# Performance work log

Measured on AMD Instinct MI355X. Metric: run time of the kernel, lower is better.

The kernel has to match this reference:

```python
import jax, jax.numpy as jnp
import numpy as np

EPS = 1e-12  # F.normalize default eps


def setup_inputs() -> dict:
    key = jax.random.key(0)
    k1, k2, k3 = jax.random.split(key, 3)
    B, C, H, W = 4, 64, 64, 64
    background = jax.random.normal(k1, (B, C, H, W), dtype=jnp.float32)
    foreground = jax.random.normal(k2, (B, C, H, W), dtype=jnp.float32)
    # binary mask, broadcast over channels
    mask = jnp.round(jax.random.uniform(k3, (B, 1, H, W), dtype=jnp.float32))
    return {"background": background, "foreground": foreground, "mask": mask}


def _l2norm(x, axis):
    # matches torch F.normalize: x / max(||x||, eps)
    n = jnp.sqrt(jnp.sum(x * x, axis=axis, keepdims=True))
    return x / jnp.maximum(n, EPS)


def reference(background, foreground, mask):
    B, C, H, W = background.shape
    bg_flat = background.reshape(B, C, H * W)   # [B, C, K]
    fg_flat = foreground.reshape(B, C, H * W)   # [B, C, Q]
    norm_bg = _l2norm(bg_flat, axis=1)
    norm_fg = _l2norm(fg_flat, axis=1)
    # cosine-similarity scores [B, K, Q]
    attention = jnp.einsum('bck,bcq->bkq', norm_bg, norm_fg)
    attention = jax.nn.softmax(attention, axis=1)  # over bg (key) axis
    attended = jnp.einsum('bck,bkq->bcq', bg_flat, attention)
    attended = attended.reshape(B, C, H, W)
    return foreground * (1.0 - mask) + attended * mask
```

## Files before the change

### kernel.cpp

```cpp
#include <hip/hip_runtime.h>
#include <math.h>

#define CC 64
#define HWN 4096
#define QB 32
#define KSPLIT 4
#define KT 32
#define NCH (HWN / KSPLIT / KT)

typedef __attribute__((ext_vector_type(8))) short bf16x8;
typedef __attribute__((ext_vector_type(4))) float f32x4;

__device__ __align__(16) unsigned short g_bgT[4][HWN][CC];
__device__ __align__(16) unsigned short g_bgN[4][CC][HWN];
__device__ __align__(16) unsigned short g_fgT[4][HWN][CC];

static __device__ __forceinline__ unsigned int f2bf(float x) {
  union { float f; unsigned int u; } v; v.f = x;
  return (v.u + 0x7fffu + ((v.u >> 16) & 1u)) >> 16;
}
static __device__ __forceinline__ unsigned int packbf(float lo, float hi) {
  return f2bf(lo) | (f2bf(hi) << 16);
}

__global__ __launch_bounds__(256) void prep_kernel(const float* __restrict__ bg,
                                                   const float* __restrict__ fg) {
  __shared__ float lds[64 * 65];
  const int bid = blockIdx.x;
  const int kt = bid & 63, b = (bid >> 6) & 3, which = bid >> 8;
  const float* src = (which ? fg : bg) + (size_t)b * CC * HWN + kt * 64;
  const int tid = threadIdx.x;

  {
    int c = tid >> 2, k0 = (tid & 3) * 16;
#pragma unroll
    for (int j4 = 0; j4 < 4; ++j4) {
      float4 v = *(const float4*)(src + (size_t)c * HWN + k0 + 4 * j4);
      lds[(k0 + 4 * j4 + 0) * 65 + c] = v.x;
      lds[(k0 + 4 * j4 + 1) * 65 + c] = v.y;
      lds[(k0 + 4 * j4 + 2) * 65 + c] = v.z;
      lds[(k0 + 4 * j4 + 3) * 65 + c] = v.w;
    }
  }
  __syncthreads();

  const int k = tid >> 2, u = tid & 3;
  float ss = 0.f;
#pragma unroll
  for (int j = 0; j < 16; ++j) {
    float v = lds[k * 65 + u * 16 + j];
    ss = fmaf(v, v, ss);
  }
  ss += __shfl_xor(ss, 1, 64);
  ss += __shfl_xor(ss, 2, 64);
  const float s = 1.0f / fmaxf(sqrtf(ss), 1e-12f);

  {
    unsigned int* gT32 = (unsigned int*)(which ? &g_fgT[0][0][0] : &g_bgT[0][0][0]);
    size_t R = (size_t)b * HWN + kt * 64 + k;
    unsigned int w8[8];
#pragma unroll
    for (int i = 0; i < 8; ++i) {
      int c2 = u * 16 + 2 * i;
      w8[i] = packbf(lds[k * 65 + c2] * s, lds[k * 65 + c2 + 1] * s);
    }
    *(uint4*)&gT32[R * 32 + u * 8]     = make_uint4(w8[0], w8[1], w8[2], w8[3]);
    *(uint4*)&gT32[R * 32 + u * 8 + 4] = make_uint4(w8[4], w8[5], w8[6], w8[7]);
  }

  if (which == 0) {
    unsigned int* gN32 = (unsigned int*)&g_bgN[0][0][0];
    int cN = tid >> 2, vN = tid & 3;
    unsigned int n8[8];
#pragma unroll
    for (int i = 0; i < 8; ++i) {
      int kk = vN * 16 + 2 * i;
      n8[i] = packbf(lds[kk * 65 + cN], lds[(kk + 1) * 65 + cN]);
    }
    size_t RN = ((size_t)b * CC + cN) * (HWN / 2) + kt * 32 + vN * 8;
    *(uint4*)&gN32[RN]     = make_uint4(n8[0], n8[1], n8[2], n8[3]);
    *(uint4*)&gN32[RN + 4] = make_uint4(n8[4], n8[5], n8[6], n8[7]);
  }
}

#define P_OFF 65536
#define ML_OFF 75776
#define SMEM_BYTES 76288
__global__ __launch_bounds__(256, 2) void attn_kernel(const float* __restrict__ fg,
                                                      const float* __restrict__ mask,
                                                      float* __restrict__ out) {
  __shared__ __align__(16) char smem[SMEM_BYTES];
  const int b = blockIdx.y;
  const int q0 = blockIdx.x * QB;
  const int tid = threadIdx.x;
  const int lane = tid & 63;
  const int ks = tid >> 6;
  const int m16 = lane & 15;
  const int quad = lane >> 4;

  bf16x8 Bf[2][2];
#pragma unroll
  for (int qf = 0; qf < 2; ++qf)
#pragma unroll
    for (int h = 0; h < 2; ++h)
      Bf[qf][h] = *(const bf16x8*)&g_fgT[b][q0 + qf * 16 + m16][h * 32 + quad * 8];

  const unsigned short* srcT[4];
  const unsigned short* srcN[4];
  int offT[4];
  int offN[4];
#pragma unroll
  for (int t = 0; t < 4; ++t) {
    int ub = t * 64;
    int uT = ub + lane;
    int kk = uT >> 3, pos = uT & 7, j = pos ^ (kk & 7);
    srcT[t] = &g_bgT[b][ks * 1024 + kk][j * 8];
    offT[t] = ks * 8192 + ub * 16;
    int cc = uT >> 2, pos4 = uT & 3, j4 = pos4 ^ ((cc >> 1) & 3);
    srcN[t] = &g_bgN[b][cc][ks * 1024 + j4 * 8];
    offN[t] = ks * 8192 + 4096 + ub * 16;
  }

  unsigned short* P = (unsigned short*)(smem + P_OFF + ks * 2560);
  float* mL = (float*)(smem + ML_OFF);

  float l_run[2] = {0.f, 0.f};
  f32x4 O[4][2];
#pragma unroll
  for (int t = 0; t < 4; ++t)
#pragma unroll
    for (int qf = 0; qf < 2; ++qf) O[t][qf] = (f32x4){0.f, 0.f, 0.f, 0.f};

  const int posN = quad ^ ((m16 >> 1) & 3);

  auto stage = [&](int bufoff) {
#pragma unroll
    for (int t = 0; t < 4; ++t) {
      __builtin_amdgcn_global_load_lds(
          (const __attribute__((address_space(1))) unsigned int*)srcT[t],
          (__attribute__((address_space(3))) unsigned int*)(smem + bufoff + offT[t]), 16, 0, 0);
      __builtin_amdgcn_global_load_lds(
          (const __attribute__((address_space(1))) unsigned int*)srcN[t],
          (__attribute__((address_space(3))) unsigned int*)(smem + bufoff + offN[t]), 16, 0, 0);
      srcT[t] += KT * CC;
      srcN[t] += KT;
    }
  };

  stage(0);

  int buf = 0;
  for (int it = 0; it < NCH; ++it) {
    if (it + 1 < NCH) {
      stage(buf ^ 32768);
      asm volatile("s_waitcnt vmcnt(8)" ::: "memory");
    } else {
      asm volatile("s_waitcnt vmcnt(0)" ::: "memory");
    }

    const char* baseT = smem + buf + ks * 8192;
    const char* baseN = baseT + 4096;

    f32x4 S[2][2];
    __builtin_amdgcn_s_setprio(1);
#pragma unroll
    for (int i = 0; i < 2; ++i) {
      int kk = 16 * i + m16;
      bf16x8 A0 = *(const bf16x8*)(baseT + kk * 128 + ((quad) ^ (kk & 7)) * 16);
      bf16x8 A1 = *(const bf16x8*)(baseT + kk * 128 + ((4 + quad) ^ (kk & 7)) * 16);
#pragma unroll
      for (int qf = 0; qf < 2; ++qf) {
        f32x4 acc = {0.f, 0.f, 0.f, 0.f};
        acc = __builtin_amdgcn_mfma_f32_16x16x32_bf16(A0, Bf[qf][0], acc, 0, 0, 0);
        acc = __builtin_amdgcn_mfma_f32_16x16x32_bf16(A1, Bf[qf][1], acc, 0, 0, 0);
        S[qf][i] = acc;
      }
    }
    __builtin_amdgcn_s_setprio(0);

#pragma unroll
    for (int qf = 0; qf < 2; ++qf) {
      float pe[2][4];
      float ps = 0.f;
#pragma unroll
      for (int i = 0; i < 2; ++i)
#pragma unroll
        for (int r = 0; r < 4; ++r) {
          pe[i][r] = __expf(S[qf][i][r] - 1.0f);
          ps += pe[i][r];
        }
      ps += __shfl_xor(ps, 16, 64);
      ps += __shfl_xor(ps, 32, 64);
      l_run[qf] += ps;
#pragma unroll
      for (int i = 0; i < 2; ++i) {
        union { float f; unsigned int u; } x0, x1, x2, x3;
        x0.f = pe[i][0]; x1.f = pe[i][1]; x2.f = pe[i][2]; x3.f = pe[i][3];
        unsigned int p01 = __builtin_amdgcn_perm(x1.u + 0x8000u, x0.u + 0x8000u, 0x07060302u);
        unsigned int p23 = __builtin_amdgcn_perm(x3.u + 0x8000u, x2.u + 0x8000u, 0x07060302u);
        *(uint2*)&P[(qf * 16 + m16) * 40 + 16 * i + quad * 4] = make_uint2(p01, p23);
      }
    }

    bf16x8 Pf0 = *(const bf16x8*)&P[m16 * 40 + quad * 8];
    bf16x8 Pf1 = *(const bf16x8*)&P[(16 + m16) * 40 + quad * 8];
    __builtin_amdgcn_s_setprio(1);
#pragma unroll
    for (int t = 0; t < 4; ++t) {
      int c = 16 * t + m16;
      bf16x8 A = *(const bf16x8*)(baseN + c * 64 + posN * 16);
      O[t][0] = __builtin_amdgcn_mfma_f32_16x16x32_bf16(A, Pf0, O[t][0], 0, 0, 0);
      O[t][1] = __builtin_amdgcn_mfma_f32_16x16x32_bf16(A, Pf1, O[t][1], 0, 0, 0);
    }
    __builtin_amdgcn_s_setprio(0);

    buf ^= 32768;
  }

  if (quad == 0) {
    mL[ks * 32 + m16] = l_run[0];
    mL[ks * 32 + 16 + m16] = l_run[1];
  }
  __syncthreads();
  float* mO = (float*)smem;
#pragma unroll
  for (int t = 0; t < 4; ++t)
#pragma unroll
    for (int qf = 0; qf < 2; ++qf)
#pragma unroll
      for (int r = 0; r < 4; ++r)
        mO[(ks * 64 + 16 * t + quad * 4 + r) * 34 + qf * 16 + m16] = O[t][qf][r];
  __syncthreads();
  {
    const float* fgB = fg + (size_t)b * CC * HWN;
    const float* mk = mask + (size_t)b * HWN;
    float* outB = out + (size_t)b * CC * HWN;
    int q = tid & 31, cb = tid >> 5;
    int qglob = q0 + q;
    float L = mL[0 * 32 + q] + mL[1 * 32 + q] + mL[2 * 32 + q] + mL[3 * 32 + q];
    float invL = 1.0f / L;
    float mv = mk[qglob];
#pragma unroll
    for (int e = 0; e < 8; ++e) {
      int c = cb * 8 + e;
      float acc = mO[(0 * 64 + c) * 34 + q] + mO[(1 * 64 + c) * 34 + q] +
                  mO[(2 * 64 + c) * 34 + q] + mO[(3 * 64 + c) * 34 + q];
      float att = acc * invL;
      float fgv = fgB[(size_t)c * HWN + qglob];
      outB[(size_t)c * HWN + qglob] = fgv + mv * (att - fgv);
    }
  }
}

extern "C" void kernel_launch(void* const* d_in, const int* in_sizes, int n_in,
                              void* d_out, int out_size, void* d_ws, size_t ws_size,
                              hipStream_t stream) {
  const float* background = (const float*)d_in[0];
  const float* foreground = (const float*)d_in[1];
  const float* mask       = (const float*)d_in[2];
  float* out = (float*)d_out;
  prep_kernel<<<512, 256, 0, stream>>>(background, foreground);
  attn_kernel<<<dim3(HWN / QB, 4), 256, 0, stream>>>(foreground, mask, out);
}
```

Before: 105.5 us.

## Halve query tile, load bgN fragments directly to registers, swizzle block order

Shrinks the query tile from 32 to 16 and cuts LDS use so four workgroups can share a CU. The channel-major background operand is now loaded straight from global memory into register double-buffers instead of being staged through LDS. A 1D grid with an XCD-aware block remap is added, and the softmax row-sum shuffle reduction moves out of the loop to run once at the end. Each block now does half the work per loaded background tile, so total global/L2 traffic for the background doubles in exchange for more parallelism and occupancy.

```diff
diff --git a/kernel.cpp b/kernel.cpp
--- a/kernel.cpp
+++ b/kernel.cpp
@@ -3,7 +3,7 @@
 
 #define CC 64
 #define HWN 4096
-#define QB 32
+#define QB 16
 #define KSPLIT 4
 #define KT 32
 #define NCH (HWN / KSPLIT / KT)
@@ -83,168 +83,146 @@
   }
 }
 
-#define P_OFF 65536
-#define ML_OFF 75776
-#define SMEM_BYTES 76288
-__global__ __launch_bounds__(256, 2) void attn_kernel(const float* __restrict__ fg,
+#define P_OFF 32768
+#define ML_OFF 37888
+#define SMEM_BYTES 38144
+__global__ __launch_bounds__(256, 4) void attn_kernel(const float* __restrict__ fg,
                                                       const float* __restrict__ mask,
                                                       float* __restrict__ out) {
   __shared__ __align__(16) char smem[SMEM_BYTES];
-  const int b = blockIdx.y;
-  const int q0 = blockIdx.x * QB;
+  const int wg = blockIdx.x;
+  const int wgp = (wg & 7) * 128 + (wg >> 3);
+  const int b = wgp >> 8;
+  const int q0 = (wgp & 255) * QB;
   const int tid = threadIdx.x;
   const int lane = tid & 63;
   const int ks = tid >> 6;
   const int m16 = lane & 15;
   const int quad = lane >> 4;
 
-  bf16x8 Bf[2][2];
-#pragma unroll
-  for (int qf = 0; qf < 2; ++qf)
-#pragma unroll
-    for (int h = 0; h < 2; ++h)
-      Bf[qf][h] = *(const bf16x8*)&g_fgT[b][q0 + qf * 16 + m16][h * 32 + quad * 8];
+  bf16x8 Bf[2];
+#pragma unroll
+  for (int h = 0; h < 2; ++h)
+    Bf[h] = *(const bf16x8*)&g_fgT[b][q0 + m16][h * 32 + quad * 8];
 
   const unsigned short* srcT[4];
-  const unsigned short* srcN[4];
   int offT[4];
-  int offN[4];
 #pragma unroll
   for (int t = 0; t < 4; ++t) {
-    int ub = t * 64;
-    int uT = ub + lane;
+    int uT = t * 64 + lane;
     int kk = uT >> 3, pos = uT & 7, j = pos ^ (kk & 7);
     srcT[t] = &g_bgT[b][ks * 1024 + kk][j * 8];
-    offT[t] = ks * 8192 + ub * 16;
-    int cc = uT >> 2, pos4 = uT & 3, j4 = pos4 ^ ((cc >> 1) & 3);
-    srcN[t] = &g_bgN[b][cc][ks * 1024 + j4 * 8];
-    offN[t] = ks * 8192 + 4096 + ub * 16;
-  }
-
-  unsigned short* P = (unsigned short*)(smem + P_OFF + ks * 2560);
+    offT[t] = ks * 4096 + t * 1024;
+  }
+
+  const unsigned short* pN = &g_bgN[b][m16][ks * 1024 + quad * 8];
+
+  unsigned short* P = (unsigned short*)(smem + P_OFF + ks * 1280);
   float* mL = (float*)(smem + ML_OFF);
 
-  float l_run[2] = {0.f, 0.f};
-  f32x4 O[4][2];
-#pragma unroll
-  for (int t = 0; t < 4; ++t)
-#pragma unroll
-    for (int qf = 0; qf < 2; ++qf) O[t][qf] = (f32x4){0.f, 0.f, 0.f, 0.f};
-
-  const int posN = quad ^ ((m16 >> 1) & 3);
-
-  auto stage = [&](int bufoff) {
+  float l_run = 0.f;
+  f32x4 O[4];
+#pragma unroll
+  for (int t = 0; t < 4; ++t) O[t] = (f32x4){0.f, 0.f, 0.f, 0.f};
+
+  auto stageT = [&](int bufoff) {
 #pragma unroll
     for (int t = 0; t < 4; ++t) {
       __builtin_amdgcn_global_load_lds(
           (const __attribute__((address_space(1))) unsigned int*)srcT[t],
           (__attribute__((address_space(3))) unsigned int*)(smem + bufoff + offT[t]), 16, 0, 0);
-      __builtin_amdgcn_global_load_lds(
-          (const __attribute__((address_space(1))) unsigned int*)srcN[t],
-          (__attribute__((address_space(3))) unsigned int*)(smem + bufoff + offN[t]), 16, 0, 0);
       srcT[t] += KT * CC;
-      srcN[t] += KT;
     }
   };
 
-  stage(0);
-
-  int buf = 0;
-  for (int it = 0; it < NCH; ++it) {
+  bf16x8 A0r[4], A1r[4];
+  auto loadN = [&](bf16x8 (&A)[4], int ch) {
+#pragma unroll
+    for (int t = 0; t < 4; ++t)
+      A[t] = *(const bf16x8*)(pN + (size_t)t * 16 * HWN + (size_t)ch * KT);
+  };
+
+  auto iter = [&](int it, int co, int no, bf16x8 (&Ac)[4], bf16x8 (&An)[4]) {
     if (it + 1 < NCH) {
-      stage(buf ^ 32768);
+      stageT(no);
+      loadN(An, it + 1);
       asm volatile("s_waitcnt vmcnt(8)" ::: "memory");
     } else {
       asm volatile("s_waitcnt vmcnt(0)" ::: "memory");
     }
 
-    const char* baseT = smem + buf + ks * 8192;
-    const char* baseN = baseT + 4096;
-
-    f32x4 S[2][2];
+    const char* baseT = smem + co + ks * 4096;
+
+    f32x4 S[2];
     __builtin_amdgcn_s_setprio(1);
 #pragma unroll
     for (int i = 0; i < 2; ++i) {
       int kk = 16 * i + m16;
-      bf16x8 A0 = *(const bf16x8*)(baseT + kk * 128 + ((quad) ^ (kk & 7)) * 16);
-      bf16x8 A1 = *(const bf16x8*)(baseT + kk * 128 + ((4 + quad) ^ (kk & 7)) * 16);
-#pragma unroll
-      for (int qf = 0; qf < 2; ++qf) {
-        f32x4 acc = {0.f, 0.f, 0.f, 0.f};
-        acc = __builtin_amdgcn_mfma_f32_16x16x32_bf16(A0, Bf[qf][0], acc, 0, 0, 0);
-        acc = __builtin_amdgcn_mfma_f32_16x16x32_bf16(A1, Bf[qf][1], acc, 0, 0, 0);
-        S[qf][i] = acc;
+      bf16x8 T0 = *(const bf16x8*)(baseT + kk * 128 + ((quad) ^ (kk & 7)) * 16);
+      bf16x8 T1 = *(const bf16x8*)(baseT + kk * 128 + ((4 + quad) ^ (kk & 7)) * 16);
+      f32x4 acc = {0.f, 0.f, 0.f, 0.f};
+      acc = __builtin_amdgcn_mfma_f32_16x16x32_bf16(T0, Bf[0], acc, 0, 0, 0);
+      acc = __builtin_amdgcn_mfma_f32_16x16x32_bf16(T1, Bf[1], acc, 0, 0, 0);
+      S[i] = acc;
+    }
+    __builtin_amdgcn_s_setprio(0);
+
+#pragma unroll
+    for (int i = 0; i < 2; ++i) {
+      float pe[4];
+#pragma unroll
+      for (int r = 0; r < 4; ++r) {
+        pe[r] = __expf(S[i][r] - 1.0f);
+        l_run += pe[r];
       }
-    }
+      union { float f; unsigned int u; } x0, x1, x2, x3;
+      x0.f = pe[0]; x1.f = pe[1]; x2.f = pe[2]; x3.f = pe[3];
+      unsigned int p01 = __builtin_amdgcn_perm(x1.u + 0x8000u, x0.u + 0x8000u, 0x07060302u);
+      unsigned int p23 = __builtin_amdgcn_perm(x3.u + 0x8000u, x2.u + 0x8000u, 0x07060302u);
+      *(uint2*)&P[m16 * 40 + 16 * i + quad * 4] = make_uint2(p01, p23);
+    }
+
+    bf16x8 Pf = *(const bf16x8*)&P[m16 * 40 + quad * 8];
+    __builtin_amdgcn_s_setprio(1);
+#pragma unroll
+    for (int t = 0; t < 4; ++t)
+      O[t] = __builtin_amdgcn_mfma_f32_16x16x32_bf16(Ac[t], Pf, O[t], 0, 0, 0);
     __builtin_amdgcn_s_setprio(0);
-
-#pragma unroll
-    for (int qf = 0; qf < 2; ++qf) {
-      float pe[2][4];
-      float ps = 0.f;
-#pragma unroll
-      for (int i = 0; i < 2; ++i)
-#pragma unroll
-        for (int r = 0; r < 4; ++r) {
-          pe[i][r] = __expf(S[qf][i][r] - 1.0f);
-          ps += pe[i][r];
-        }
-      ps += __shfl_xor(ps, 16, 64);
-      ps += __shfl_xor(ps, 32, 64);
-      l_run[qf] += ps;
-#pragma unroll
-      for (int i = 0; i < 2; ++i) {
-        union { float f; unsigned int u; } x0, x1, x2, x3;
-        x0.f = pe[i][0]; x1.f = pe[i][1]; x2.f = pe[i][2]; x3.f = pe[i][3];
-        unsigned int p01 = __builtin_amdgcn_perm(x1.u + 0x8000u, x0.u + 0x8000u, 0x07060302u);
-        unsigned int p23 = __builtin_amdgcn_perm(x3.u + 0x8000u, x2.u + 0x8000u, 0x07060302u);
-        *(uint2*)&P[(qf * 16 + m16) * 40 + 16 * i + quad * 4] = make_uint2(p01, p23);
-      }
-    }
-
-    bf16x8 Pf0 = *(const bf16x8*)&P[m16 * 40 + quad * 8];
-    bf16x8 Pf1 = *(const bf16x8*)&P[(16 + m16) * 40 + quad * 8];
-    __builtin_amdgcn_s_setprio(1);
-#pragma unroll
-    for (int t = 0; t < 4; ++t) {
-      int c = 16 * t + m16;
-      bf16x8 A = *(const bf16x8*)(baseN + c * 64 + posN * 16);
-      O[t][0] = __builtin_amdgcn_mfma_f32_16x16x32_bf16(A, Pf0, O[t][0], 0, 0, 0);
-      O[t][1] = __builtin_amdgcn_mfma_f32_16x16x32_bf16(A, Pf1, O[t][1], 0, 0, 0);
-    }
-    __builtin_amdgcn_s_setprio(0);
-
-    buf ^= 32768;
-  }
-
-  if (quad == 0) {
-    mL[ks * 32 + m16] = l_run[0];
-    mL[ks * 32 + 16 + m16] = l_run[1];
-  }
+  };
+
+  stageT(0);
+  loadN(A0r, 0);
+
+  for (int it2 = 0; it2 < NCH; it2 += 2) {
+    iter(it2,     0,     16384, A0r, A1r);
+    iter(it2 + 1, 16384, 0,     A1r, A0r);
+  }
+
+  l_run += __shfl_xor(l_run, 16, 64);
+  l_run += __shfl_xor(l_run, 32, 64);
+  if (quad == 0) mL[ks * 16 + m16] = l_run;
   __syncthreads();
   float* mO = (float*)smem;
 #pragma unroll
   for (int t = 0; t < 4; ++t)
 #pragma unroll
-    for (int qf = 0; qf < 2; ++qf)
-#pragma unroll
-      for (int r = 0; r < 4; ++r)
-        mO[(ks * 64 + 16 * t + quad * 4 + r) * 34 + qf * 16 + m16] = O[t][qf][r];
+    for (int r = 0; r < 4; ++r)
+      mO[(ks * 64 + 16 * t + quad * 4 + r) * 17 + m16] = O[t][r];
   __syncthreads();
   {
     const float* fgB = fg + (size_t)b * CC * HWN;
     const float* mk = mask + (size_t)b * HWN;
     float* outB = out + (size_t)b * CC * HWN;
-    int q = tid & 31, cb = tid >> 5;
+    int q = tid & 15, cb = tid >> 4;
     int qglob = q0 + q;
-    float L = mL[0 * 32 + q] + mL[1 * 32 + q] + mL[2 * 32 + q] + mL[3 * 32 + q];
+    float L = mL[0 * 16 + q] + mL[1 * 16 + q] + mL[2 * 16 + q] + mL[3 * 16 + q];
     float invL = 1.0f / L;
     float mv = mk[qglob];
 #pragma unroll
-    for (int e = 0; e < 8; ++e) {
-      int c = cb * 8 + e;
-      float acc = mO[(0 * 64 + c) * 34 + q] + mO[(1 * 64 + c) * 34 + q] +
-                  mO[(2 * 64 + c) * 34 + q] + mO[(3 * 64 + c) * 34 + q];
+    for (int e = 0; e < 4; ++e) {
+      int c = cb * 4 + e;
+      float acc = mO[(0 * 64 + c) * 17 + q] + mO[(1 * 64 + c) * 17 + q] +
+                  mO[(2 * 64 + c) * 17 + q] + mO[(3 * 64 + c) * 17 + q];
       float att = acc * invL;
       float fgv = fgB[(size_t)c * HWN + qglob];
       outB[(size_t)c * HWN + qglob] = fgv + mv * (att - fgv);
@@ -260,5 +238,5 @@
   const float* mask       = (const float*)d_in[2];
   float* out = (float*)d_out;
   prep_kernel<<<512, 256, 0, stream>>>(background, foreground);
-  attn_kernel<<<dim3(HWN / QB, 4), 256, 0, stream>>>(foreground, mask, out);
-}
+  attn_kernel<<<dim3(HWN / QB * 4), 256, 0, stream>>>(foreground, mask, out);
+}
```

Measured after the change: 141.4 us. 1.34x slower.
